# Kernel tuning notes

Hardware: AMD Instinct MI355X
Metric: run time of the kernel (lower is better)

## Reference

```python
import jax, jax.numpy as jnp
import numpy as np

T, D, K = 16384, 512, 128
NODES = [512, 512]


def _rnn_layer(X, Wx, Wh, bh, h0):
    # X: [T, M1] -> [T, M2]; precompute input projection (parallel part)
    Xp = X @ Wx  # [T, M2]
    def step(h, x):
        h = jax.nn.relu(x + h @ Wh + bh)
        return h, h
    _, out = jax.lax.scan(step, h0[0], Xp)
    return out  # [T, M2]


def setup_inputs() -> dict:
    key = jax.random.key(0)
    ks = jax.random.split(key, 16)
    inp = {"X": jax.random.normal(ks[0], (T, D), dtype=jnp.float32)}
    M1 = D
    for i, M2 in enumerate(NODES):
        s = 1.0 / np.sqrt(M1 + M2)
        inp[f"Wx{i}"] = jax.random.normal(ks[1 + 3 * i], (M1, M2), dtype=jnp.float32) * s
        inp[f"Wh{i}"] = jax.random.normal(ks[2 + 3 * i], (M2, M2), dtype=jnp.float32) * s
        inp[f"bh{i}"] = jnp.zeros((M2,), dtype=jnp.float32)
        inp[f"h0{i}"] = jnp.zeros((1, M2), dtype=jnp.float32)
        M1 = M2
    # nn.Linear(M1, K): weight [K, M1], bias [K]
    lim = 1.0 / np.sqrt(M1)
    inp["W_log"] = jax.random.uniform(ks[10], (K, M1), minval=-lim, maxval=lim, dtype=jnp.float32)
    inp["b_log"] = jax.random.uniform(ks[11], (K,), minval=-lim, maxval=lim, dtype=jnp.float32)
    return inp


def reference(X, Wx0, Wh0, bh0, h00, Wx1, Wh1, bh1, h01, W_log, b_log):
    h = _rnn_layer(X, Wx0, Wh0, bh0, h00)
    h = _rnn_layer(h, Wx1, Wh1, bh1, h01)
    return h @ W_log.T + b_log  # [T, K]
```

## Files before the change

kernel.cpp:

```cpp
#include <hip/hip_runtime.h>
#include <stdint.h>

#define TT 16384
#define DH 512
#define KK 128
#define SENT 0xAAAAAAAAu
#define CROWS 32
#define NCHUNK (TT / CROWS)
#define NPROJ 56
#define RSLOT 16

__device__ uint32_t g_ring[2][RSLOT][DH];
__device__ uint32_t g_flagXp[2][NCHUNK];

static __device__ __forceinline__ uint32_t aload(const uint32_t* p) {
    return __hip_atomic_load(p, __ATOMIC_RELAXED, __HIP_MEMORY_SCOPE_AGENT);
}
static __device__ __forceinline__ void astore(uint32_t* p, uint32_t v) {
    __hip_atomic_store(p, v, __ATOMIC_RELAXED, __HIP_MEMORY_SCOPE_AGENT);
}
static __device__ __forceinline__ float aloadf(const float* p) {
    return __uint_as_float(aload((const uint32_t*)p));
}

__global__ void init_kernel() {
    const int tid = threadIdx.x;
    uint32_t* r = &g_ring[0][0][0];
    for (int i = tid; i < 2 * RSLOT * DH; i += 1024) r[i] = SENT;
    uint32_t* f = &g_flagXp[0][0];
    for (int i = tid; i < 2 * NCHUNK; i += 1024) f[i] = SENT;
}

static __device__ void proj_chunk(const float* __restrict__ W,
                                  const float* __restrict__ src, int srcMode,
                                  float* __restrict__ dst, uint32_t* flag, int t0,
                                  float* inT , float* wt )
{
    const int tid = threadIdx.x;
    #pragma unroll
    for (int i = 0; i < 16; ++i) {
        int idx = tid + 1024 * i;
        int row = idx >> 9;
        int col = idx & 511;
        float v;
        if (srcMode == 0) {
            v = src[(size_t)t0 * DH + idx];
        } else {
            const uint32_t* p = (const uint32_t*)src + (size_t)t0 * DH + idx;
            uint32_t u;
            while ((u = aload(p)) == SENT) __builtin_amdgcn_s_sleep(1);
            v = __uint_as_float(u);
        }
        inT[col * 36 + row] = v;
    }
    __syncthreads();

    const int rg = (tid >> 7) & 7;
    const int cg = tid & 127;
    float acc[4][4] = {{0.f}};

    for (int kt = 0; kt < 16; ++kt) {
        const int k0 = kt * 32;
        #pragma unroll
        for (int i = 0; i < 4; ++i) {
            int f4 = tid + 1024 * i;
            int wr = f4 >> 7;
            int wc = (f4 & 127) << 2;
            *(float4*)&wt[wr * 516 + wc] =
                *(const float4*)&W[(size_t)(k0 + wr) * DH + wc];
        }
        __syncthreads();
        #pragma unroll 8
        for (int kk = 0; kk < 32; ++kk) {
            float4 a = *(const float4*)&inT[(k0 + kk) * 36 + (rg << 2)];
            float4 w = *(const float4*)&wt[kk * 516 + (cg << 2)];
            acc[0][0] += a.x * w.x; acc[0][1] += a.x * w.y; acc[0][2] += a.x * w.z; acc[0][3] += a.x * w.w;
            acc[1][0] += a.y * w.x; acc[1][1] += a.y * w.y; acc[1][2] += a.y * w.z; acc[1][3] += a.y * w.w;
            acc[2][0] += a.z * w.x; acc[2][1] += a.z * w.y; acc[2][2] += a.z * w.z; acc[2][3] += a.z * w.w;
            acc[3][0] += a.w * w.x; acc[3][1] += a.w * w.y; acc[3][2] += a.w * w.z; acc[3][3] += a.w * w.w;
        }
        __syncthreads();
    }
    #pragma unroll
    for (int i = 0; i < 4; ++i)
        #pragma unroll
        for (int j = 0; j < 4; ++j)
            astore((uint32_t*)&dst[(size_t)(t0 + (rg << 2) + i) * DH + (cg << 2) + j],
                   __float_as_uint(acc[i][j]));
    __threadfence();
    __syncthreads();
    if (tid == 0)
        __hip_atomic_store(flag, 1u, __ATOMIC_RELEASE, __HIP_MEMORY_SCOPE_AGENT);
}

__global__ __launch_bounds__(1024, 1)
void fused(const float* __restrict__ X,
           const float* __restrict__ Wx0, const float* __restrict__ Wh0,
           const float* __restrict__ bh0, const float* __restrict__ h00,
           const float* __restrict__ Wx1, const float* __restrict__ Wh1,
           const float* __restrict__ bh1, const float* __restrict__ h01,
           float* H0r, float* H1r)
{
    __shared__ __align__(16) float s_hbuf[DH];
    __shared__ float s_part[8][128];
    __shared__ __align__(16) float s_inT[DH * 36];
    __shared__ __align__(16) float s_wt[32 * 516];

    const int bIdx = blockIdx.x;
    const int m8 = bIdx & 7;
    const int tid = threadIdx.x;

    if (bIdx < 32 && m8 < 2) {
        const int L = m8;
        const int b = bIdx >> 3;
        const int c = tid >> 7;
        const int o = tid & 127;
        const int og = (b << 7) + o;

        const float* Wh  = L ? Wh1 : Wh0;
        const float* bhv = L ? bh1 : bh0;
        const float* h0v = L ? h01 : h00;
        float* Hful      = L ? H1r : H0r;
        const float* Xp  = L ? H0r : H1r;
        uint32_t* ring         = &g_ring[L][0][0];
        uint32_t* flagXp       = &g_flagXp[L][0];

        float wh[64];
        #pragma unroll
        for (int j = 0; j < 64; ++j)
            wh[j] = Wh[(size_t)((c << 6) + j) * DH + og];
        const float bias = bhv[og];

        const int ptid = (tid + 1024 - ((b << 8) + 256)) & 1023;
        const bool isPoll = ptid < 384;
        const int pcol = (ptid < (b << 7)) ? ptid : ptid + 128;
        const bool isSelf = (c >> 1) == b;
        const bool isRed = tid < 128;

        if (tid < DH) s_hbuf[tid] = h0v[tid];

        float xp_next = 0.f;
        int curCh = -1;
        if (isRed) {
            while (__hip_atomic_load(&flagXp[0], __ATOMIC_ACQUIRE,
                                     __HIP_MEMORY_SCOPE_AGENT) != 1u)
                __builtin_amdgcn_s_sleep(1);
            curCh = 0;
            xp_next = aloadf(&Xp[og]);
        }
        __syncthreads();

        for (int t = 0; t < TT; ++t) {
            if (t > 0 && isPoll) {
                const uint32_t par = (uint32_t)((t - 1) >> 4) & 1u;
                const uint32_t* p = &ring[(((t - 1) & 15) << 9) + pcol];
                uint32_t v;
                do { v = aload(p); } while ((v >> 31) != par);
                s_hbuf[pcol] = __uint_as_float(v & 0x7fffffffu);
            }
            float acc = 0.f;
            if (isSelf | (t == 0)) {
                const float4* h4 = (const float4*)&s_hbuf[c << 6];
                #pragma unroll
                for (int j4 = 0; j4 < 16; ++j4) {
                    float4 hv = h4[j4];
                    acc += wh[4*j4+0]*hv.x + wh[4*j4+1]*hv.y
                         + wh[4*j4+2]*hv.z + wh[4*j4+3]*hv.w;
                }
                s_part[c][o] = acc;
            }
            __syncthreads();
            if (!(isSelf | (t == 0))) {
                const float4* h4 = (const float4*)&s_hbuf[c << 6];
                #pragma unroll
                for (int j4 = 0; j4 < 16; ++j4) {
                    float4 hv = h4[j4];
                    acc += wh[4*j4+0]*hv.x + wh[4*j4+1]*hv.y
                         + wh[4*j4+2]*hv.z + wh[4*j4+3]*hv.w;
                }
                s_part[c][o] = acc;
            }
            __syncthreads();
            if (isRed) {
                float v = bias + xp_next;
                #pragma unroll
                for (int cc = 0; cc < 8; ++cc) v += s_part[cc][o];
                v = fmaxf(v, 0.f);
                const uint32_t hb = __float_as_uint(v);
                astore(&ring[((t & 15) << 9) + og],
                       hb | (((uint32_t)(t >> 4) & 1u) << 31));
                astore((uint32_t*)Hful + (size_t)t * DH + og, hb);
                s_hbuf[og] = v;
                if (t + 1 < TT) {
                    const int ch = (t + 1) >> 5;
                    if (ch != curCh) {
                        while (__hip_atomic_load(&flagXp[ch], __ATOMIC_ACQUIRE,
                                                 __HIP_MEMORY_SCOPE_AGENT) != 1u) {}
                        curCh = ch;
                    }
                    xp_next = aloadf(&Xp[(size_t)(t + 1) * DH + og]);
                }
            }
            __syncthreads();
        }
    } else {
        const int pi = (bIdx < 32) ? (((bIdx >> 3) * 6) + (m8 - 2))
                                   : (24 + (bIdx - 32));
        for (int cc = pi; cc < NCHUNK; cc += NPROJ) {
            proj_chunk(Wx0, X,   0, H1r , &g_flagXp[0][cc], cc * CROWS, s_inT, s_wt);
            proj_chunk(Wx1, H0r, 1, H0r , &g_flagXp[1][cc], cc * CROWS, s_inT, s_wt);
        }
    }
}

__global__ __launch_bounds__(128, 1)
void logits_kernel(const float* __restrict__ H1, const float* __restrict__ Wl,
                   const float* __restrict__ bl, float* __restrict__ out)
{
    const int t0 = blockIdx.x * 8;
    const int k = threadIdx.x;

    __shared__ __align__(16) float hs[8 * DH];
    for (int idx = k; idx < 8 * DH / 4; idx += 128)
        ((float4*)hs)[idx] = ((const float4*)&H1[(size_t)t0 * DH])[idx];
    __syncthreads();

    float acc[8];
    const float bk = bl[k];
    #pragma unroll
    for (int r = 0; r < 8; ++r) acc[r] = bk;

    const float4* w4 = (const float4*)&Wl[(size_t)k * DH];
    for (int j = 0; j < DH / 4; ++j) {
        float4 w = w4[j];
        #pragma unroll
        for (int r = 0; r < 8; ++r) {
            float4 h = ((const float4*)&hs[r * DH])[j];
            acc[r] += w.x * h.x + w.y * h.y + w.z * h.z + w.w * h.w;
        }
    }
    #pragma unroll
    for (int r = 0; r < 8; ++r) out[(size_t)(t0 + r) * KK + k] = acc[r];
}

extern "C" void kernel_launch(void* const* d_in, const int* in_sizes, int n_in,
                              void* d_out, int out_size, void* d_ws, size_t ws_size,
                              hipStream_t stream)
{
    const float* X   = (const float*)d_in[0];
    const float* Wx0 = (const float*)d_in[1];
    const float* Wh0 = (const float*)d_in[2];
    const float* bh0 = (const float*)d_in[3];
    const float* h00 = (const float*)d_in[4];
    const float* Wx1 = (const float*)d_in[5];
    const float* Wh1 = (const float*)d_in[6];
    const float* bh1 = (const float*)d_in[7];
    const float* h01 = (const float*)d_in[8];
    const float* Wl  = (const float*)d_in[9];
    const float* bl  = (const float*)d_in[10];
    float* out = (float*)d_out;

    float* H0r = (float*)d_ws;
    float* H1r = H0r + (size_t)TT * DH;

    hipMemsetAsync(d_ws, 0xAA, (size_t)TT * DH * sizeof(float), stream);
    hipLaunchKernelGGL(init_kernel, dim3(1), dim3(1024), 0, stream);
    hipLaunchKernelGGL(fused, dim3(64), dim3(1024), 0, stream,
                       X, Wx0, Wh0, bh0, h00, Wx1, Wh1, bh1, h01, H0r, H1r);
    hipLaunchKernelGGL(logits_kernel, dim3(TT / 8), dim3(128), 0, stream,
                       H1r, Wl, bl, out);
}
```

Before: 20.13 ms.

## Split RNN scan across 8 blocks per layer with wave-level flag reduction instead of barriers

The recurrent scan now uses 8 blocks of 512 threads per layer, each owning 64 output columns, instead of 4 blocks of 1024 threads. Each wave reads its 64-element slice of the previous hidden state directly from the global ring. Wave 0 gathers partial sums from the other waves through LDS flags, which removes the per-step __syncthreads barriers. The projection workers double to 112 blocks with a 4x8 register tile and share LDS through a union. This shortens the per-step critical path but doubles cross-block polling traffic and relies on intra-workgroup spin-waits being safe.

```diff
diff --git a/kernel.cpp b/kernel.cpp
--- a/kernel.cpp
+++ b/kernel.cpp
@@ -7,7 +7,7 @@
 #define SENT 0xAAAAAAAAu
 #define CROWS 32
 #define NCHUNK (TT / CROWS)
-#define NPROJ 56
+#define NPROJ 112
 #define RSLOT 16
 
 __device__ uint32_t g_ring[2][RSLOT][DH];
@@ -31,15 +31,19 @@
     for (int i = tid; i < 2 * NCHUNK; i += 1024) f[i] = SENT;
 }
 
-static __device__ void proj_chunk(const float* __restrict__ W,
+union __align__(16) SMem {
+    struct { float inT[DH * 36]; float wt[32 * 516]; } proj;
+    struct { float ch[8][64]; float part[2][8][64]; uint32_t flag[8]; } scan;
+};
+
+static __device__ void proj_chunk(SMem& sm, const float* __restrict__ W,
                                   const float* __restrict__ src, int srcMode,
-                                  float* __restrict__ dst, uint32_t* flag, int t0,
-                                  float* inT , float* wt )
+                                  float* __restrict__ dst, uint32_t* flag, int t0)
 {
     const int tid = threadIdx.x;
     #pragma unroll
-    for (int i = 0; i < 16; ++i) {
-        int idx = tid + 1024 * i;
+    for (int i = 0; i < 32; ++i) {
+        int idx = tid + 512 * i;
         int row = idx >> 9;
         int col = idx & 511;
         float v;
@@ -51,41 +55,48 @@
             while ((u = aload(p)) == SENT) __builtin_amdgcn_s_sleep(1);
             v = __uint_as_float(u);
         }
-        inT[col * 36 + row] = v;
+        sm.proj.inT[col * 36 + row] = v;
     }
     __syncthreads();
 
-    const int rg = (tid >> 7) & 7;
-    const int cg = tid & 127;
-    float acc[4][4] = {{0.f}};
+    const int rg = tid >> 6;
+    const int cg = tid & 63;
+    float acc[4][8];
+    #pragma unroll
+    for (int i = 0; i < 4; ++i)
+        #pragma unroll
+        for (int j = 0; j < 8; ++j) acc[i][j] = 0.f;
 
     for (int kt = 0; kt < 16; ++kt) {
         const int k0 = kt * 32;
         #pragma unroll
-        for (int i = 0; i < 4; ++i) {
-            int f4 = tid + 1024 * i;
+        for (int i = 0; i < 8; ++i) {
+            int f4 = tid + 512 * i;
             int wr = f4 >> 7;
             int wc = (f4 & 127) << 2;
-            *(float4*)&wt[wr * 516 + wc] =
+            *(float4*)&sm.proj.wt[wr * 516 + wc] =
                 *(const float4*)&W[(size_t)(k0 + wr) * DH + wc];
         }
         __syncthreads();
-        #pragma unroll 8
+        #pragma unroll 4
         for (int kk = 0; kk < 32; ++kk) {
-            float4 a = *(const float4*)&inT[(k0 + kk) * 36 + (rg << 2)];
-            float4 w = *(const float4*)&wt[kk * 516 + (cg << 2)];
-            acc[0][0] += a.x * w.x; acc[0][1] += a.x * w.y; acc[0][2] += a.x * w.z; acc[0][3] += a.x * w.w;
-            acc[1][0] += a.y * w.x; acc[1][1] += a.y * w.y; acc[1][2] += a.y * w.z; acc[1][3] += a.y * w.w;
-            acc[2][0] += a.z * w.x; acc[2][1] += a.z * w.y; acc[2][2] += a.z * w.z; acc[2][3] += a.z * w.w;
-            acc[3][0] += a.w * w.x; acc[3][1] += a.w * w.y; acc[3][2] += a.w * w.z; acc[3][3] += a.w * w.w;
+            float4 a  = *(const float4*)&sm.proj.inT[(k0 + kk) * 36 + (rg << 2)];
+            float4 w0 = *(const float4*)&sm.proj.wt[kk * 516 + (cg << 3)];
+            float4 w1 = *(const float4*)&sm.proj.wt[kk * 516 + (cg << 3) + 4];
+            float av[4] = {a.x, a.y, a.z, a.w};
+            float wv[8] = {w0.x, w0.y, w0.z, w0.w, w1.x, w1.y, w1.z, w1.w};
+            #pragma unroll
+            for (int i = 0; i < 4; ++i)
+                #pragma unroll
+                for (int j = 0; j < 8; ++j) acc[i][j] += av[i] * wv[j];
         }
         __syncthreads();
     }
     #pragma unroll
     for (int i = 0; i < 4; ++i)
         #pragma unroll
-        for (int j = 0; j < 4; ++j)
-            astore((uint32_t*)&dst[(size_t)(t0 + (rg << 2) + i) * DH + (cg << 2) + j],
+        for (int j = 0; j < 8; ++j)
+            astore((uint32_t*)&dst[(size_t)(t0 + (rg << 2) + i) * DH + (cg << 3) + j],
                    __float_as_uint(acc[i][j]));
     __threadfence();
     __syncthreads();
@@ -93,7 +104,7 @@
         __hip_atomic_store(flag, 1u, __ATOMIC_RELEASE, __HIP_MEMORY_SCOPE_AGENT);
 }
 
-__global__ __launch_bounds__(1024, 1)
+__global__ __launch_bounds__(512, 1)
 void fused(const float* __restrict__ X,
            const float* __restrict__ Wx0, const float* __restrict__ Wh0,
            const float* __restrict__ bh0, const float* __restrict__ h00,
@@ -101,96 +112,82 @@
            const float* __restrict__ bh1, const float* __restrict__ h01,
            float* H0r, float* H1r)
 {
-    __shared__ __align__(16) float s_hbuf[DH];
-    __shared__ float s_part[8][128];
-    __shared__ __align__(16) float s_inT[DH * 36];
-    __shared__ __align__(16) float s_wt[32 * 516];
-
+    __shared__ SMem sm;
     const int bIdx = blockIdx.x;
-    const int m8 = bIdx & 7;
     const int tid = threadIdx.x;
 
-    if (bIdx < 32 && m8 < 2) {
-        const int L = m8;
-        const int b = bIdx >> 3;
-        const int c = tid >> 7;
-        const int o = tid & 127;
-        const int og = (b << 7) + o;
+    if (bIdx < 16) {
+        const int L     = bIdx & 1;
+        const int slice = bIdx >> 1;
+        const int w     = tid >> 6;
+        const int lane  = tid & 63;
+        const int colg  = (slice << 6) + lane;
+        const int q     = (slice + w) & 7;
 
         const float* Wh  = L ? Wh1 : Wh0;
         const float* bhv = L ? bh1 : bh0;
         const float* h0v = L ? h01 : h00;
         float* Hful      = L ? H1r : H0r;
         const float* Xp  = L ? H0r : H1r;
-        uint32_t* ring         = &g_ring[L][0][0];
-        uint32_t* flagXp       = &g_flagXp[L][0];
+        uint32_t* ring   = &g_ring[L][0][0];
+        uint32_t* flagXp = &g_flagXp[L][0];
 
         float wh[64];
         #pragma unroll
         for (int j = 0; j < 64; ++j)
-            wh[j] = Wh[(size_t)((c << 6) + j) * DH + og];
-        const float bias = bhv[og];
-
-        const int ptid = (tid + 1024 - ((b << 8) + 256)) & 1023;
-        const bool isPoll = ptid < 384;
-        const int pcol = (ptid < (b << 7)) ? ptid : ptid + 128;
-        const bool isSelf = (c >> 1) == b;
-        const bool isRed = tid < 128;
-
-        if (tid < DH) s_hbuf[tid] = h0v[tid];
-
-        float xp_next = 0.f;
-        int curCh = -1;
-        if (isRed) {
+            wh[j] = Wh[(size_t)((q << 6) + j) * DH + colg];
+        const float bias = bhv[colg];
+
+        if (tid < 8) sm.scan.flag[tid] = 0;
+        __syncthreads();
+
+        float v_prev = 0.f, xp_cur = 0.f;
+        int curCh = 0;
+        if (w == 0) {
+            v_prev = h0v[colg];
             while (__hip_atomic_load(&flagXp[0], __ATOMIC_ACQUIRE,
-                                     __HIP_MEMORY_SCOPE_AGENT) != 1u)
-                __builtin_amdgcn_s_sleep(1);
-            curCh = 0;
-            xp_next = aloadf(&Xp[og]);
-        }
-        __syncthreads();
+                                     __HIP_MEMORY_SCOPE_AGENT) != 1u) {}
+            xp_cur = aloadf(&Xp[colg]);
+        }
 
         for (int t = 0; t < TT; ++t) {
-            if (t > 0 && isPoll) {
+            float h;
+            if (w == 0) {
+                h = v_prev;
+            } else if (t == 0) {
+                h = h0v[(q << 6) + lane];
+            } else {
                 const uint32_t par = (uint32_t)((t - 1) >> 4) & 1u;
-                const uint32_t* p = &ring[(((t - 1) & 15) << 9) + pcol];
-                uint32_t v;
-                do { v = aload(p); } while ((v >> 31) != par);
-                s_hbuf[pcol] = __uint_as_float(v & 0x7fffffffu);
+                const uint32_t* p = &ring[(((t - 1) & 15) << 9) + (q << 6) + lane];
+                uint32_t u;
+                do { u = aload(p); } while ((u >> 31) != par);
+                h = __uint_as_float(u & 0x7fffffffu);
             }
+            sm.scan.ch[w][lane] = h;
             float acc = 0.f;
-            if (isSelf | (t == 0)) {
-                const float4* h4 = (const float4*)&s_hbuf[c << 6];
-                #pragma unroll
-                for (int j4 = 0; j4 < 16; ++j4) {
-                    float4 hv = h4[j4];
-                    acc += wh[4*j4+0]*hv.x + wh[4*j4+1]*hv.y
-                         + wh[4*j4+2]*hv.z + wh[4*j4+3]*hv.w;
+            const float4* h4 = (const float4*)sm.scan.ch[w];
+            #pragma unroll
+            for (int j = 0; j < 16; ++j) {
+                float4 hv = h4[j];
+                acc += wh[4*j+0]*hv.x + wh[4*j+1]*hv.y
+                     + wh[4*j+2]*hv.z + wh[4*j+3]*hv.w;
+            }
+
+            if (w == 0) {
+                float sum = bias + xp_cur + acc;
+                const int par = t & 1;
+                for (int ww = 1; ww < 8; ++ww) {
+                    while (__hip_atomic_load(&sm.scan.flag[ww], __ATOMIC_ACQUIRE,
+                                             __HIP_MEMORY_SCOPE_WORKGROUP)
+                           < (uint32_t)(t + 1)) {}
+                    sum += sm.scan.part[par][ww][lane];
                 }
-                s_part[c][o] = acc;
-            }
-            __syncthreads();
-            if (!(isSelf | (t == 0))) {
-                const float4* h4 = (const float4*)&s_hbuf[c << 6];
-                #pragma unroll
-                for (int j4 = 0; j4 < 16; ++j4) {
-                    float4 hv = h4[j4];
-                    acc += wh[4*j4+0]*hv.x + wh[4*j4+1]*hv.y
-                         + wh[4*j4+2]*hv.z + wh[4*j4+3]*hv.w;
-                }
-                s_part[c][o] = acc;
-            }
-            __syncthreads();
-            if (isRed) {
-                float v = bias + xp_next;
-                #pragma unroll
-                for (int cc = 0; cc < 8; ++cc) v += s_part[cc][o];
-                v = fmaxf(v, 0.f);
+                float v = fmaxf(sum, 0.f);
                 const uint32_t hb = __float_as_uint(v);
-                astore(&ring[((t & 15) << 9) + og],
-                       hb | (((uint32_t)(t >> 4) & 1u) << 31));
-                astore((uint32_t*)Hful + (size_t)t * DH + og, hb);
-                s_hbuf[og] = v;
+                astore(&ring[((t & 15) << 9) + colg],
+                       hb | ((uint32_t)((t >> 4) & 1u) << 31));
+                astore((uint32_t*)&Hful[(size_t)t * DH + colg], hb);
+                v_prev = v;
                 if (t + 1 < TT) {
                     const int ch = (t + 1) >> 5;
                     if (ch != curCh) {
@@ -198,17 +195,20 @@
                                                  __HIP_MEMORY_SCOPE_AGENT) != 1u) {}
                         curCh = ch;
                     }
-                    xp_next = aloadf(&Xp[(size_t)(t + 1) * DH + og]);
+                    xp_cur = aloadf(&Xp[(size_t)(t + 1) * DH + colg]);
                 }
+            } else {
+                sm.scan.part[t & 1][w][lane] = acc;
+                if (lane == 0)
+                    __hip_atomic_store(&sm.scan.flag[w], (uint32_t)(t + 1),
+                                       __ATOMIC_RELEASE, __HIP_MEMORY_SCOPE_WORKGROUP);
             }
-            __syncthreads();
         }
     } else {
-        const int pi = (bIdx < 32) ? (((bIdx >> 3) * 6) + (m8 - 2))
-                                   : (24 + (bIdx - 32));
+        const int pi = bIdx - 16;
         for (int cc = pi; cc < NCHUNK; cc += NPROJ) {
-            proj_chunk(Wx0, X,   0, H1r , &g_flagXp[0][cc], cc * CROWS, s_inT, s_wt);
-            proj_chunk(Wx1, H0r, 1, H0r , &g_flagXp[1][cc], cc * CROWS, s_inT, s_wt);
+            proj_chunk(sm, Wx0, X,   0, H1r , &g_flagXp[0][cc], cc * CROWS);
+            proj_chunk(sm, Wx1, H0r, 1, H0r , &g_flagXp[1][cc], cc * CROWS);
         }
     }
 }
@@ -265,7 +265,7 @@
 
     hipMemsetAsync(d_ws, 0xAA, (size_t)TT * DH * sizeof(float), stream);
     hipLaunchKernelGGL(init_kernel, dim3(1), dim3(1024), 0, stream);
-    hipLaunchKernelGGL(fused, dim3(64), dim3(1024), 0, stream,
+    hipLaunchKernelGGL(fused, dim3(16 + NPROJ), dim3(512), 0, stream,
                        X, Wx0, Wh0, bh0, h00, Wx1, Wh1, bh1, h01, H0r, H1r);
     hipLaunchKernelGGL(logits_kernel, dim3(TT / 8), dim3(128), 0, stream,
                        H1r, Wl, bl, out);
```

Measured after the change: 25.37 ms. +26.0%, slower.
